# Optimization experiments

Measured on AMD Instinct MI355X. Metric: run time of the kernel, lower is better.

Reference implementation:

```python
import jax, jax.numpy as jnp
import numpy as np
from jax import lax

MIN_DELTA = 0.5 / 2 ** 3  # COMPATIBLE = False path
MAX_STEP = 20
MAX_CAMSTEP = 6
# (name, n_options, action_range_start) for non-camera discrete actions.
# range_start follows the original: commit=[0,1], camera=[1,6], then cumulative n-1.
ACTS = [("forward_back", 3, 6), ("left_right", 3, 8), ("jump", 2, 10),
        ("sneak_sprint", 4, 11), ("attack", 32, 14)]
N_ACTIONS = 45  # 6 + sum(n-1) = 6 + 39


def _forward(fc_input, camera, acts, W1, b1, W2, b2):
    B = fc_input.shape[0]
    dt = fc_input.dtype
    cam0, cam1 = camera[:, 0], camera[:, 1]
    acts = {k: v.astype(jnp.int32) for k, v in acts.items()}

    def step(carry, _):
        ac, delta, chosen, rdac, cam_steps, commited = carry
        alive = ~commited  # loss mask for this step (norm accounting in original)
        # build fc0 extra input: [current_ac(2), one-hots(44), delta(1), delta_chosen(1)]
        parts = [ac]
        for name, n, lo in ACTS:
            parts.append(jax.nn.one_hot(rdac[name], n, dtype=dt))
        step_in = jnp.concatenate(parts + [delta[:, None], chosen.astype(dt)[:, None]], axis=1)

        # ---- target dac computation (torch.no_grad block) ----
        commit = ((jnp.abs(cam0) < 1e-5) & (jnp.abs(cam1) < 1e-5)) | (cam_steps >= MAX_CAMSTEP)
        for name, n, lo in ACTS:
            commit = commit & (rdac[name] == acts[name])
        dac = jnp.zeros((B,), jnp.int32)
        modified = commit
        new_rdac = {}
        for name, n, lo in ACTS:
            a = acts[name]
            r = rdac[name]
            disc = (~modified) & (r != a)
            val = jnp.where(a == 0, r - 1 + lo, a - 1 + lo).astype(jnp.int32)
            dac = jnp.where(disc, val, dac)
            new_rdac[name] = jnp.where(disc, a, r)
            modified = modified | disc
        ac0, ac1 = ac[:, 0], ac[:, 1]
        # NOTE: original compares both camera components against ac[:, 0] (faithful).
        delta_mask = (~modified) & (~chosen) & (
            (jnp.abs(cam0 - ac0) > delta * 2.0) | (jnp.abs(cam1 - ac0) > delta * 2.0))
        dac = jnp.where(delta_mask, 5, dac)
        delta = jnp.where(delta_mask, jnp.clip(delta * 2.0, -0.5, 0.5), delta)
        modified = modified | delta_mask
        m = ~modified
        incX = cam0 >= ac0
        incY = cam1 >= ac1
        # quadrants: decX&decY->1, incX&decY->2, decX&incY->3, incX&incY->4
        dac = jnp.where(m, 1 + incX.astype(jnp.int32) + 2 * incY.astype(jnp.int32), dac)
        sx = jnp.where(incX, delta, -delta)
        sy = jnp.where(incY, delta, -delta)
        ac = jnp.stack([jnp.where(m, ac0 + sx, ac0), jnp.where(m, ac1 + sy, ac1)], axis=1)
        delta = jnp.where(m, delta * 0.5, delta)
        chosen = chosen | m
        cam_steps = cam_steps + m.astype(jnp.int32)
        commited = commited | commit
        return (ac, delta, chosen, new_rdac, cam_steps, commited), (step_in, dac, alive)

    init = (jnp.zeros((B, 2), dt),
            jnp.full((B,), MIN_DELTA, dt),
            jnp.zeros((B,), bool),
            {name: jnp.zeros((B,), jnp.int32) for name, _, _ in ACTS},
            jnp.zeros((B,), jnp.int32),
            jnp.zeros((B,), bool))
    _, (step_ins, dacs, alives) = lax.scan(step, init, None, length=MAX_STEP)
    # step_ins: [T,B,48], dacs: [T,B], alives: [T,B]
    T = MAX_STEP
    x = jnp.concatenate(
        [jnp.broadcast_to(fc_input[None], (T,) + fc_input.shape), step_ins], axis=-1)
    x = x.reshape(T * B, -1)
    h = x @ W1 + b1
    h = h * jax.nn.sigmoid(h)  # swish
    logits = h @ W2 + b2
    logp = jax.nn.log_softmax(logits, axis=-1)
    ce = -jnp.take_along_axis(logp, dacs.reshape(-1, 1), axis=1)[:, 0].reshape(T, B)
    af = alives.astype(ce.dtype)
    loss = (ce * af).sum(0) / af.sum(0)  # per-sample loss normalized by #active steps
    return loss.mean()


def setup_inputs() -> dict:
    key = jax.random.key(0)
    ks = jax.random.split(key, 10)
    B, NI, H = 4096, 1024, 2048
    D_IN = NI + 4 + 44  # 1072
    return {
        "fc_input": jax.random.normal(ks[0], (B, NI), jnp.float32),
        "camera": jax.random.normal(ks[1], (B, 2), jnp.float32),
        "forward_back": jax.random.randint(ks[2], (B,), 0, 3),
        "left_right": jax.random.randint(ks[3], (B,), 0, 3),
        "jump": jax.random.randint(ks[4], (B,), 0, 2),
        "sneak_sprint": jax.random.randint(ks[5], (B,), 0, 4),
        "attack": jax.random.randint(ks[6], (B,), 0, 32),
        "W1": jax.random.normal(ks[7], (D_IN, H), jnp.float32) * 0.02,
        "b1": jnp.zeros((H,), jnp.float32),
        "W2": jax.random.normal(ks[8], (H, N_ACTIONS), jnp.float32) * 0.02,
        "b2": jnp.zeros((N_ACTIONS,), jnp.float32),
    }


def reference(fc_input, camera, forward_back, left_right, jump, sneak_sprint, attack,
              W1, b1, W2, b2):
    acts = {"forward_back": forward_back, "left_right": left_right, "jump": jump,
            "sneak_sprint": sneak_sprint, "attack": attack}
    return _forward(fc_input, camera, acts, W1, b1, W2, b2)
```

## Files before the change

### kernel.cpp

```cpp
#include <hip/hip_runtime.h>

#define BATCH 4096
#define NI 1024
#define HID 2048
#define TSTEPS 20
#define NA 45
#define TW 512
#define SROW 520
#define MAXS 16
#define NB 4

typedef __bf16 bf16x8 __attribute__((ext_vector_type(8)));
typedef float floatx4 __attribute__((ext_vector_type(4)));

struct StepMeta {
    float ac0, ac1, delta, chosen;
    int chg;
    int dac, mult, pad;
};

__device__ __forceinline__ unsigned short f2bf(float x) {
    union { float f; unsigned int u; } un; un.f = x;
    unsigned int r = un.u + 0x7FFFu + ((un.u >> 16) & 1u);
    return (unsigned short)(r >> 16);
}

__device__ __forceinline__ float4 f4add(float4 a, float4 b) {
    return make_float4(a.x + b.x, a.y + b.y, a.z + b.z, a.w + b.w);
}

__device__ void scan_one(int b, const float* __restrict__ camera,
                         const int* __restrict__ fb_in, const int* __restrict__ lr_in,
                         const int* __restrict__ jp_in, const int* __restrict__ ss_in,
                         const int* __restrict__ at_in, StepMeta* __restrict__ meta,
                         int2* __restrict__ hdr) {
    float cam0 = camera[2 * b], cam1 = camera[2 * b + 1];
    int afb = fb_in[b], alr = lr_in[b], ajp = jp_in[b], ass = ss_in[b], aat = at_in[b];
    float ac0 = 0.f, ac1 = 0.f, delta = 0.0625f;
    int rfb = 0, rlr = 0, rjp = 0, rss = 0, rat = 0;
    bool chosen = false;
    int cam_steps = 0;
    int chgPending = -1;
    bool camzero = (fabsf(cam0) < 1e-5f) && (fabsf(cam1) < 1e-5f);
    int nd = 0, aliveTot = 0;
    float lac0 = 0.f, lac1 = 0.f, ldelta = 0.f, lchosen = 0.f;
    int ldac = -1000;
    for (int t = 0; t < TSTEPS; t++) {
        StepMeta m;
        m.ac0 = ac0; m.ac1 = ac1; m.delta = delta; m.chosen = chosen ? 1.f : 0.f;
        m.chg = chgPending; chgPending = -1;
        bool commit = (camzero || cam_steps >= 6) &&
                      rfb == afb && rlr == alr && rjp == ajp && rss == ass && rat == aat;
        int dac = 0; bool modified = commit;
        if (!modified && rfb != afb) { dac = (afb == 0 ? rfb - 1 + 6  : afb - 1 + 6 ); chgPending = ((2  + rfb) << 8) | (2  + afb); rfb = afb; modified = true; }
        if (!modified && rlr != alr) { dac = (alr == 0 ? rlr - 1 + 8  : alr - 1 + 8 ); chgPending = ((5  + rlr) << 8) | (5  + alr); rlr = alr; modified = true; }
        if (!modified && rjp != ajp) { dac = (ajp == 0 ? rjp - 1 + 10 : ajp - 1 + 10); chgPending = ((8  + rjp) << 8) | (8  + ajp); rjp = ajp; modified = true; }
        if (!modified && rss != ass) { dac = (ass == 0 ? rss - 1 + 11 : ass - 1 + 11); chgPending = ((10 + rss) << 8) | (10 + ass); rss = ass; modified = true; }
        if (!modified && rat != aat) { dac = (aat == 0 ? rat - 1 + 14 : aat - 1 + 14); chgPending = ((14 + rat) << 8) | (14 + aat); rat = aat; modified = true; }
        if (!modified && !chosen &&
            (fabsf(cam0 - ac0) > delta * 2.f || fabsf(cam1 - ac0) > delta * 2.f)) {
            dac = 5; delta = fminf(delta * 2.f, 0.5f); modified = true;
        }
        if (!modified) {
            bool incX = cam0 >= ac0, incY = cam1 >= ac1;
            dac = 1 + (incX ? 1 : 0) + (incY ? 2 : 0);
            ac0 += incX ? delta : -delta;
            ac1 += incY ? delta : -delta;
            delta *= 0.5f;
            chosen = true;
            cam_steps++;
        }
        m.dac = dac; m.mult = 1; m.pad = 0;
        if (nd > 0 && m.chg < 0 && !commit &&
            m.ac0 == lac0 && m.ac1 == lac1 && m.delta == ldelta &&
            m.chosen == lchosen && dac == ldac) {
            meta[b * MAXS + nd - 1].mult = 1 + (TSTEPS - t);
            aliveTot += (TSTEPS - t);
            break;
        }
        meta[b * MAXS + nd] = m;
        lac0 = m.ac0; lac1 = m.ac1; ldelta = m.delta; lchosen = m.chosen; ldac = dac;
        nd++; aliveTot++;
        if (commit) break;
    }
    hdr[b] = make_int2(nd, aliveTot);
}

__global__ void prep_kernel(const float* __restrict__ fc, unsigned short* __restrict__ Ab,
                            const float* __restrict__ W1, unsigned short* __restrict__ Wt,
                            const float* __restrict__ W2, unsigned short* __restrict__ W2T,
                            const float* __restrict__ camera,
                            const int* __restrict__ fb_in, const int* __restrict__ lr_in,
                            const int* __restrict__ jp_in, const int* __restrict__ ss_in,
                            const int* __restrict__ at_in, StepMeta* __restrict__ meta,
                            int2* __restrict__ hdr) {
    __shared__ float tile[32][33];
    int bid = blockIdx.x, tid = threadIdx.x;
    if (bid < 4096) {
        int idx = bid * 256 + tid;
        float4 v = ((const float4*)fc)[idx];
        ushort4 o;
        o.x = f2bf(v.x); o.y = f2bf(v.y); o.z = f2bf(v.z); o.w = f2bf(v.w);
        ((ushort4*)Ab)[idx] = o;
    } else if (bid < 6144) {
        int b2 = bid - 4096;
        int k0 = (b2 & 31) * 32, n0 = (b2 >> 5) * 32;
        int tx = tid & 31, ty = tid >> 5;
        for (int i = 0; i < 4; i++)
            tile[ty + 8 * i][tx] = W1[(size_t)(k0 + ty + 8 * i) * HID + n0 + tx];
        __syncthreads();
        for (int i = 0; i < 4; i++) {
            int n = ty + 8 * i;
            Wt[(size_t)(n0 + n) * NI + k0 + tx] = f2bf(tile[tx][n]);
        }
    } else if (bid < 6272) {
        int bid2 = bid - 6144;
        int k = bid2 * 16 + (tid >> 4);
        int nn = tid & 15;
#pragma unroll
        for (int i = 0; i < 3; i++) {
            int n = nn * 3 + i;
            W2T[(size_t)n * HID + k] = (n < NA) ? f2bf(W2[(size_t)k * NA + n]) : (unsigned short)0;
        }
    } else {
        int b = (bid - 6272) * 256 + tid;
        scan_one(b, camera, fb_in, lr_in, jp_in, ss_in, at_in, meta, hdr);
    }
}

__global__ __launch_bounds__(256) void gemm_base(const unsigned short* __restrict__ Ab,
                                                 const unsigned short* __restrict__ Wt,
                                                 const float* __restrict__ W1,
                                                 const float* __restrict__ b1,
                                                 float* __restrict__ C) {
    __shared__ __align__(16) __bf16 At[128 * 64];
    __shared__ __align__(16) __bf16 Bt[64 * 64];
    int bn = blockIdx.x, bm = blockIdx.y;
    int m0 = bm * 128, n0 = bn * 64;
    int tid = threadIdx.x;
    int wave = tid >> 6, lane = tid & 63;
    int wr = wave >> 1, wc = wave & 1;
    int l15 = lane & 15, q = lane >> 4;
    floatx4 acc[4][2];
    for (int a = 0; a < 4; a++) for (int c = 0; c < 2; c++) acc[a][c] = (floatx4){0.f, 0.f, 0.f, 0.f};
    for (int k0 = 0; k0 < NI; k0 += 64) {
        __syncthreads();
#pragma unroll
        for (int i = 0; i < 4; i++) {
            int c = i * 256 + tid;
            int row = c >> 3;
            int part = (c & 7) ^ (row & 7);
            const unsigned short* gA = &Ab[(size_t)(m0 + row) * NI + k0 + part * 8];
            __builtin_amdgcn_global_load_lds(
                (const __attribute__((address_space(1))) unsigned int*)gA,
                (__attribute__((address_space(3))) unsigned int*)&At[c * 8], 16, 0, 0);
        }
#pragma unroll
        for (int i = 0; i < 2; i++) {
            int c = i * 256 + tid;
            int row = c >> 3;
            int part = (c & 7) ^ (row & 7);
            const unsigned short* gB = &Wt[(size_t)(n0 + row) * NI + k0 + part * 8];
            __builtin_amdgcn_global_load_lds(
                (const __attribute__((address_space(1))) unsigned int*)gB,
                (__attribute__((address_space(3))) unsigned int*)&Bt[c * 8], 16, 0, 0);
        }
        __syncthreads();
#pragma unroll
        for (int ks = 0; ks < 2; ks++) {
            bf16x8 af[4], bf[2];
            for (int mr = 0; mr < 4; mr++) {
                int row = wr * 64 + mr * 16 + l15;
                int idx = (row * 64 + ks * 32 + q * 8) ^ ((row & 7) << 3);
                af[mr] = *(const bf16x8*)&At[idx];
            }
            for (int nc = 0; nc < 2; nc++) {
                int row = wc * 32 + nc * 16 + l15;
                int idx = (row * 64 + ks * 32 + q * 8) ^ ((row & 7) << 3);
                bf[nc] = *(const bf16x8*)&Bt[idx];
            }
            for (int mr = 0; mr < 4; mr++)
                for (int nc = 0; nc < 2; nc++)
                    acc[mr][nc] = __builtin_amdgcn_mfma_f32_16x16x32_bf16(af[mr], bf[nc], acc[mr][nc], 0, 0, 0);
        }
    }
    for (int nc = 0; nc < 2; nc++) {
        int col = n0 + wc * 32 + nc * 16 + l15;
        const float* We = W1 + (size_t)NI * HID + col;
        float cv = b1[col] + We[2 * HID] + We[5 * HID] + We[8 * HID] + We[10 * HID]
                 + We[14 * HID] + 0.0625f * We[46 * HID];
        for (int mr = 0; mr < 4; mr++)
            for (int r = 0; r < 4; r++) {
                int row = m0 + wr * 64 + mr * 16 + q * 4 + r;
                C[(size_t)row * HID + col] = acc[mr][nc][r] + cv;
            }
    }
}

__global__ __launch_bounds__(512, 2) void fused_mlp(const float* __restrict__ base,
                                                 const float* __restrict__ W1,
                                                 const unsigned short* __restrict__ W2T,
                                                 const float* __restrict__ b2,
                                                 const StepMeta* __restrict__ meta,
                                                 const int2* __restrict__ hdr,
                                                 float* __restrict__ loss_out) {
    __shared__ __align__(16) __bf16 S[NB * MAXS * SROW];
    __shared__ __align__(16) float4 u4s[NB][MAXS];
    __shared__ int chgs[NB][MAXS], dacsS[NB][MAXS], multsS[NB][MAXS];
    __shared__ int swapL[NB][5], nsS[NB], ndS[NB], atS[NB];
    __shared__ float b2s[48];
    __shared__ float ceArr[NB][MAXS];
    __shared__ float pmax[NB][MAXS][12], psum[NB][MAXS][12], mxS[NB][MAXS];

    int bp = blockIdx.x, tid = threadIdx.x;
    int tg = tid >> 7, tl = tid & 127;
    int wave = tid >> 6, lane = tid & 63, l15 = lane & 15, q = lane >> 4;

    if (tl == 0) {
        int2 hd = hdr[bp * NB + tg];
        ndS[tg] = hd.x; atS[tg] = hd.y;
    }
    if (tl < MAXS) {
        StepMeta m = meta[(size_t)(bp * NB + tg) * MAXS + tl];
        u4s[tg][tl] = make_float4(m.ac0, m.ac1, m.delta - 0.0625f, m.chosen);
        chgs[tg][tl] = m.chg; dacsS[tg][tl] = m.dac; multsS[tg][tl] = m.mult;
    }
    if (tid >= 64 && tid < 112) {
        int n = tid - 64;
        b2s[n] = (n < NA) ? b2[n] : 0.f;
    }
    __syncthreads();
    if (tl == 0) {
        int ns = 0, nd = ndS[tg];
        for (int s = 0; s < nd; s++)
            if (chgs[tg][s] >= 0) swapL[tg][ns++] = chgs[tg][s];
        nsS[tg] = ns;
        for (; ns < 5; ns++) swapL[tg][ns] = 0;
    }
    {
        uint4 zz = make_uint4(0, 0, 0, 0);
#pragma unroll
        for (int e = 0; e < NB; e++) {
            int nde = ndS[e];
            uint4* z = (uint4*)&S[(size_t)(e * MAXS + nde) * SROW];
            int n16 = (MAXS - nde) * 65;
            for (int i = tid; i < n16; i += 512) z[i] = zz;
        }
    }
    __syncthreads();

    const float* Wx = W1 + (size_t)NI * HID;
    const __bf16* Wb = (const __bf16*)W2T;
    floatx4 acc[4][3];
    for (int a = 0; a < 4; a++) for (int c = 0; c < 3; c++) acc[a][c] = (floatx4){0.f, 0.f, 0.f, 0.f};

    int nd = __builtin_amdgcn_readfirstlane(ndS[tg]);
    int ns = __builtin_amdgcn_readfirstlane(nsS[tg]);
    int cA = __builtin_amdgcn_readfirstlane(swapL[tg][0]);
    int cB = __builtin_amdgcn_readfirstlane(swapL[tg][1]);
    int cC = __builtin_amdgcn_readfirstlane(swapL[tg][2]);
    int cD = __builtin_amdgcn_readfirstlane(swapL[tg][3]);
    int cE = __builtin_amdgcn_readfirstlane(swapL[tg][4]);

    for (int jt = 0; jt < 4; jt++) {
        if (jt) __syncthreads();
        int j = jt * TW + 4 * tl;
        float4 w0  = *(const float4*)&Wx[j];
        float4 w1  = *(const float4*)&Wx[HID + j];
        float4 wdl = *(const float4*)&Wx[46 * HID + j];
        float4 wch = *(const float4*)&Wx[47 * HID + j];
        float4 hb  = *(const float4*)&base[(size_t)(bp * NB + tg) * HID + j];
        float4 dA = {0,0,0,0}, dB = {0,0,0,0}, dC = {0,0,0,0}, dD = {0,0,0,0}, dE = {0,0,0,0};
        if (ns > 0) { float4 n_ = *(const float4*)&Wx[(size_t)(cA & 255) * HID + j], o_ = *(const float4*)&Wx[(size_t)(cA >> 8) * HID + j];
                      dA = make_float4(n_.x - o_.x, n_.y - o_.y, n_.z - o_.z, n_.w - o_.w); }
        if (ns > 1) { float4 n_ = *(const float4*)&Wx[(size_t)(cB & 255) * HID + j], o_ = *(const float4*)&Wx[(size_t)(cB >> 8) * HID + j];
                      dB = make_float4(n_.x - o_.x, n_.y - o_.y, n_.z - o_.z, n_.w - o_.w); }
        if (ns > 2) { float4 n_ = *(const float4*)&Wx[(size_t)(cC & 255) * HID + j], o_ = *(const float4*)&Wx[(size_t)(cC >> 8) * HID + j];
                      dC = make_float4(n_.x - o_.x, n_.y - o_.y, n_.z - o_.z, n_.w - o_.w); }
        if (ns > 3) { float4 n_ = *(const float4*)&Wx[(size_t)(cD & 255) * HID + j], o_ = *(const float4*)&Wx[(size_t)(cD >> 8) * HID + j];
                      dD = make_float4(n_.x - o_.x, n_.y - o_.y, n_.z - o_.z, n_.w - o_.w); }
        if (ns > 4) { float4 n_ = *(const float4*)&Wx[(size_t)(cE & 255) * HID + j], o_ = *(const float4*)&Wx[(size_t)(cE >> 8) * HID + j];
                      dE = make_float4(n_.x - o_.x, n_.y - o_.y, n_.z - o_.z, n_.w - o_.w); }

        auto compute1 = [&](int s, float4 b) {
            float4 u = u4s[tg][s];
            float h0 = fmaf(u.w, wch.x, fmaf(u.x, w0.x, b.x)) + fmaf(u.z, wdl.x, u.y * w1.x);
            float h1 = fmaf(u.w, wch.y, fmaf(u.x, w0.y, b.y)) + fmaf(u.z, wdl.y, u.y * w1.y);
            float h2 = fmaf(u.w, wch.z, fmaf(u.x, w0.z, b.z)) + fmaf(u.z, wdl.z, u.y * w1.z);
            float h3 = fmaf(u.w, wch.w, fmaf(u.x, w0.w, b.w)) + fmaf(u.z, wdl.w, u.y * w1.w);
            float s0 = h0 * __builtin_amdgcn_rcpf(1.f + __expf(-h0));
            float s1 = h1 * __builtin_amdgcn_rcpf(1.f + __expf(-h1));
            float s2 = h2 * __builtin_amdgcn_rcpf(1.f + __expf(-h2));
            float s3 = h3 * __builtin_amdgcn_rcpf(1.f + __expf(-h3));
            union { uint2 v; __bf16 h[4]; } pk;
            pk.h[0] = (__bf16)s0; pk.h[1] = (__bf16)s1;
            pk.h[2] = (__bf16)s2; pk.h[3] = (__bf16)s3;
            *(uint2*)&S[(size_t)(tg * MAXS + s) * SROW + 4 * tl] = pk.v;
        };

        float4 sw = {0,0,0,0};
        compute1(0, hb);
        if (ns > 0) { sw = f4add(sw, dA); compute1(1, f4add(hb, sw)); }
        if (ns > 1) { sw = f4add(sw, dB); compute1(2, f4add(hb, sw)); }
        if (ns > 2) { sw = f4add(sw, dC); compute1(3, f4add(hb, sw)); }
        if (ns > 3) { sw = f4add(sw, dD); compute1(4, f4add(hb, sw)); }
        if (ns > 4) { sw = f4add(sw, dE); compute1(5, f4add(hb, sw)); }
        float4 bxv = f4add(hb, sw);
        int s = ns + 1;
        for (; s + 1 < nd; s += 2) {
            compute1(s, bxv);
            compute1(s + 1, bxv);
        }
        if (s < nd) compute1(s, bxv);

        __syncthreads();
#pragma unroll
        for (int i = 0; i < 2; i++) {
            int kc = (wave + 8 * i) * 32 + q * 8;
            bf16x8 a0 = *(const bf16x8*)&S[(size_t)l15 * SROW + kc];
            bf16x8 a1 = *(const bf16x8*)&S[(size_t)(MAXS + l15) * SROW + kc];
            bf16x8 a2 = *(const bf16x8*)&S[(size_t)(2 * MAXS + l15) * SROW + kc];
            bf16x8 a3 = *(const bf16x8*)&S[(size_t)(3 * MAXS + l15) * SROW + kc];
            int kg = jt * TW + kc;
            bf16x8 b0  = *(const bf16x8*)&Wb[(size_t)l15 * HID + kg];
            bf16x8 b1v = *(const bf16x8*)&Wb[(size_t)(16 + l15) * HID + kg];
            bf16x8 b2v = *(const bf16x8*)&Wb[(size_t)(32 + l15) * HID + kg];
            acc[0][0] = __builtin_amdgcn_mfma_f32_16x16x32_bf16(a0, b0,  acc[0][0], 0, 0, 0);
            acc[0][1] = __builtin_amdgcn_mfma_f32_16x16x32_bf16(a0, b1v, acc[0][1], 0, 0, 0);
            acc[0][2] = __builtin_amdgcn_mfma_f32_16x16x32_bf16(a0, b2v, acc[0][2], 0, 0, 0);
            acc[1][0] = __builtin_amdgcn_mfma_f32_16x16x32_bf16(a1, b0,  acc[1][0], 0, 0, 0);
            acc[1][1] = __builtin_amdgcn_mfma_f32_16x16x32_bf16(a1, b1v, acc[1][1], 0, 0, 0);
            acc[1][2] = __builtin_amdgcn_mfma_f32_16x16x32_bf16(a1, b2v, acc[1][2], 0, 0, 0);
            acc[2][0] = __builtin_amdgcn_mfma_f32_16x16x32_bf16(a2, b0,  acc[2][0], 0, 0, 0);
            acc[2][1] = __builtin_amdgcn_mfma_f32_16x16x32_bf16(a2, b1v, acc[2][1], 0, 0, 0);
            acc[2][2] = __builtin_amdgcn_mfma_f32_16x16x32_bf16(a2, b2v, acc[2][2], 0, 0, 0);
            acc[3][0] = __builtin_amdgcn_mfma_f32_16x16x32_bf16(a3, b0,  acc[3][0], 0, 0, 0);
            acc[3][1] = __builtin_amdgcn_mfma_f32_16x16x32_bf16(a3, b1v, acc[3][1], 0, 0, 0);
            acc[3][2] = __builtin_amdgcn_mfma_f32_16x16x32_bf16(a3, b2v, acc[3][2], 0, 0, 0);
        }
    }
    __syncthreads();
    float* logitsP = (float*)S;
    float* logitsF = (float*)S + 12288;
    if (wave >= 4) {
        int wv = wave - 4;
#pragma unroll
        for (int e = 0; e < 4; e++)
#pragma unroll
            for (int nt = 0; nt < 3; nt++)
#pragma unroll
                for (int r = 0; r < 4; r++)
                    logitsP[(size_t)(wv * 4 + e) * 768 + (q * 4 + r) * 48 + nt * 16 + l15] = acc[e][nt][r];
    }
    __syncthreads();
    if (wave < 4) {
        int wv = wave;
#pragma unroll
        for (int e = 0; e < 4; e++)
#pragma unroll
            for (int nt = 0; nt < 3; nt++)
#pragma unroll
                for (int r = 0; r < 4; r++) {
                    size_t idx = (size_t)(wv * 4 + e) * 768 + (q * 4 + r) * 48 + nt * 16 + l15;
                    logitsP[idx] += acc[e][nt][r];
                }
    }
    __syncthreads();
    for (int i = tid; i < 768; i += 512) {
        int e = i / 192, rem = i - e * 192;
        int row = rem / 12, gE = rem - row * 12;
        const float4* P0 = (const float4*)(logitsP + (size_t)(0 * 4 + e) * 768);
        const float4* P1 = (const float4*)(logitsP + (size_t)(1 * 4 + e) * 768);
        const float4* P2 = (const float4*)(logitsP + (size_t)(2 * 4 + e) * 768);
        const float4* P3 = (const float4*)(logitsP + (size_t)(3 * 4 + e) * 768);
        float4 p0 = P0[rem], p1 = P1[rem], p2 = P2[rem], p3 = P3[rem];
        float4 bb = *(const float4*)&b2s[gE * 4];
        float4 r;
        r.x = p0.x + p1.x + p2.x + p3.x + bb.x;
        r.y = p0.y + p1.y + p2.y + p3.y + bb.y;
        r.z = p0.z + p1.z + p2.z + p3.z + bb.z;
        r.w = p0.w + p1.w + p2.w + p3.w + bb.w;
        ((float4*)(logitsF + (size_t)e * 768))[rem] = r;
        float lm = (gE == 11) ? r.x : fmaxf(fmaxf(r.x, r.y), fmaxf(r.z, r.w));
        pmax[e][row][gE] = lm;
    }
    __syncthreads();
    if (tid < 64) {
        int e = tid >> 4, row = tid & 15;
        float m = pmax[e][row][0];
        for (int i = 1; i < 12; i++) m = fmaxf(m, pmax[e][row][i]);
        mxS[e][row] = m;
    }
    __syncthreads();
    for (int i = tid; i < 768; i += 512) {
        int e = i / 192, rem = i - e * 192;
        int row = rem / 12, gE = rem - row * 12;
        float m = mxS[e][row];
        float4 v = ((const float4*)(logitsF + (size_t)e * 768))[rem];
        float s;
        if (gE == 11) s = __expf(v.x - m);
        else s = __expf(v.x - m) + __expf(v.y - m) + __expf(v.z - m) + __expf(v.w - m);
        psum[e][row][gE] = s;
    }
    __syncthreads();
    if (tl < nd) {
        float ssum = 0.f;
        for (int i = 0; i < 12; i++) ssum += psum[tg][tl][i];
        float m = mxS[tg][tl];
        int dac = dacsS[tg][tl];
        float ld = logitsF[(size_t)tg * 768 + tl * 48 + dac];
        float ce = -(ld - m - logf(ssum));
        ceArr[tg][tl] = ce * (float)multsS[tg][tl];
    }
    __syncthreads();
    if (tl == 0) {
        float s = 0.f;
        for (int t = 0; t < nd; t++) s += ceArr[tg][t];
        loss_out[bp * NB + tg] = s / (float)atS[tg];
    }
}

__global__ __launch_bounds__(512) void reduce_loss(const float* __restrict__ loss,
                                                   float* __restrict__ out) {
    int tid = threadIdx.x;
    const float4* l4 = (const float4*)loss;
    float4 a = l4[tid];
    float4 b = l4[512 + tid];
    float s = (a.x + a.y + a.z + a.w) + (b.x + b.y + b.z + b.w);
    for (int off = 32; off > 0; off >>= 1) s += __shfl_down(s, off, 64);
    __shared__ float wsum[8];
    if ((tid & 63) == 0) wsum[tid >> 6] = s;
    __syncthreads();
    if (tid == 0) {
        float t = 0.f;
        for (int i = 0; i < 8; i++) t += wsum[i];
        out[0] = t * (1.0f / (float)BATCH);
    }
}

extern "C" void kernel_launch(void* const* d_in, const int* in_sizes, int n_in,
                              void* d_out, int out_size, void* d_ws, size_t ws_size,
                              hipStream_t stream) {
    const float* fc_input = (const float*)d_in[0];
    const float* camera   = (const float*)d_in[1];
    const int*   fb       = (const int*)d_in[2];
    const int*   lr       = (const int*)d_in[3];
    const int*   jp       = (const int*)d_in[4];
    const int*   ss       = (const int*)d_in[5];
    const int*   at       = (const int*)d_in[6];
    const float* W1       = (const float*)d_in[7];
    const float* b1       = (const float*)d_in[8];
    const float* W2       = (const float*)d_in[9];
    const float* b2       = (const float*)d_in[10];
    float* out = (float*)d_out;

    char* ws = (char*)d_ws;
    unsigned short* Ab   = (unsigned short*)(ws);
    unsigned short* Wt   = (unsigned short*)(ws + 8388608);
    float*          baseB= (float*)(ws + 12582912);
    StepMeta*       meta = (StepMeta*)(ws + 46137344);
    int2*           hdr  = (int2*)(ws + 48234496);
    float*          lossB= (float*)(ws + 48267264);
    unsigned short* W2T  = (unsigned short*)(ws + 48283648);

    prep_kernel<<<4096 + 2048 + 128 + 16, 256, 0, stream>>>(fc_input, Ab, W1, Wt, W2, W2T,
                                                            camera, fb, lr, jp, ss, at, meta, hdr);
    gemm_base<<<dim3(HID / 64, BATCH / 128), 256, 0, stream>>>(Ab, Wt, W1, b1, baseB);
    fused_mlp<<<BATCH / NB, 512, 0, stream>>>(baseB, W1, W2T, b2, meta, hdr, lossB);
    reduce_loss<<<1, 512, 0, stream>>>(lossB, out);
}
```

Measured before the change: 192.8 us.

## Process eight batch elements per block to amortize W2 loads

Doubles the number of batch elements handled per fused_mlp block from 4 to 8. Each thread group now builds hidden activations for two elements, and every W2T fragment loaded from global memory feeds 8 element tiles of MFMAs instead of 4. This halves the grid size and W2/W1-extra reloads per element, at the cost of doubled LDS use, more accumulator registers, and dropping to one block per CU via launch bounds.

```diff
diff --git a/kernel.cpp b/kernel.cpp
--- a/kernel.cpp
+++ b/kernel.cpp
@@ -8,7 +8,7 @@
 #define TW 512
 #define SROW 520
 #define MAXS 16
-#define NB 4
+#define NB 8
 
 typedef __bf16 bf16x8 __attribute__((ext_vector_type(8)));
 typedef float floatx4 __attribute__((ext_vector_type(4)));
@@ -197,7 +197,7 @@
     }
 }
 
-__global__ __launch_bounds__(512, 2) void fused_mlp(const float* __restrict__ base,
+__global__ __launch_bounds__(512, 1) void fused_mlp(const float* __restrict__ base,
                                                  const float* __restrict__ W1,
                                                  const unsigned short* __restrict__ W2T,
                                                  const float* __restrict__ b2,
@@ -213,30 +213,32 @@
     __shared__ float pmax[NB][MAXS][12], psum[NB][MAXS][12], mxS[NB][MAXS];
 
     int bp = blockIdx.x, tid = threadIdx.x;
-    int tg = tid >> 7, tl = tid & 127;
+    int cg = tid >> 7, ctl = tid & 127;
     int wave = tid >> 6, lane = tid & 63, l15 = lane & 15, q = lane >> 4;
 
-    if (tl == 0) {
-        int2 hd = hdr[bp * NB + tg];
-        ndS[tg] = hd.x; atS[tg] = hd.y;
-    }
-    if (tl < MAXS) {
-        StepMeta m = meta[(size_t)(bp * NB + tg) * MAXS + tl];
-        u4s[tg][tl] = make_float4(m.ac0, m.ac1, m.delta - 0.0625f, m.chosen);
-        chgs[tg][tl] = m.chg; dacsS[tg][tl] = m.dac; multsS[tg][tl] = m.mult;
+    if (tid < NB) {
+        int2 hd = hdr[bp * NB + tid];
+        ndS[tid] = hd.x; atS[tid] = hd.y;
+    }
+    if (tid >= 128 && tid < 128 + NB * MAXS) {
+        int e = (tid - 128) >> 4, s = (tid - 128) & 15;
+        StepMeta m = meta[(size_t)(bp * NB + e) * MAXS + s];
+        u4s[e][s] = make_float4(m.ac0, m.ac1, m.delta - 0.0625f, m.chosen);
+        chgs[e][s] = m.chg; dacsS[e][s] = m.dac; multsS[e][s] = m.mult;
     }
     if (tid >= 64 && tid < 112) {
         int n = tid - 64;
         b2s[n] = (n < NA) ? b2[n] : 0.f;
     }
     __syncthreads();
-    if (tl == 0) {
-        int ns = 0, nd = ndS[tg];
+    if (tid < NB) {
+        int ns = 0, nd = ndS[tid];
         for (int s = 0; s < nd; s++)
-            if (chgs[tg][s] >= 0) swapL[tg][ns++] = chgs[tg][s];
-        nsS[tg] = ns;
-        for (; ns < 5; ns++) swapL[tg][ns] = 0;
-    }
+            if (chgs[tid][s] >= 0) swapL[tid][ns++] = chgs[tid][s];
+        nsS[tid] = ns;
+        for (; ns < 5; ns++) swapL[tid][ns] = 0;
+    }
+    __syncthreads();
     {
         uint4 zz = make_uint4(0, 0, 0, 0);
 #pragma unroll
@@ -251,39 +253,30 @@
 
     const float* Wx = W1 + (size_t)NI * HID;
     const __bf16* Wb = (const __bf16*)W2T;
-    floatx4 acc[4][3];
-    for (int a = 0; a < 4; a++) for (int c = 0; c < 3; c++) acc[a][c] = (floatx4){0.f, 0.f, 0.f, 0.f};
-
-    int nd = __builtin_amdgcn_readfirstlane(ndS[tg]);
-    int ns = __builtin_amdgcn_readfirstlane(nsS[tg]);
-    int cA = __builtin_amdgcn_readfirstlane(swapL[tg][0]);
-    int cB = __builtin_amdgcn_readfirstlane(swapL[tg][1]);
-    int cC = __builtin_amdgcn_readfirstlane(swapL[tg][2]);
-    int cD = __builtin_amdgcn_readfirstlane(swapL[tg][3]);
-    int cE = __builtin_amdgcn_readfirstlane(swapL[tg][4]);
+    floatx4 acc[NB][3];
+    for (int a = 0; a < NB; a++) for (int c = 0; c < 3; c++) acc[a][c] = (floatx4){0.f, 0.f, 0.f, 0.f};
+
+    int ndA0 = __builtin_amdgcn_readfirstlane(ndS[2 * cg]);
+    int ndA1 = __builtin_amdgcn_readfirstlane(ndS[2 * cg + 1]);
+    int nsA0 = __builtin_amdgcn_readfirstlane(nsS[2 * cg]);
+    int nsA1 = __builtin_amdgcn_readfirstlane(nsS[2 * cg + 1]);
+    int cL0[5], cL1[5];
+#pragma unroll
+    for (int k = 0; k < 5; k++) {
+        cL0[k] = __builtin_amdgcn_readfirstlane(swapL[2 * cg][k]);
+        cL1[k] = __builtin_amdgcn_readfirstlane(swapL[2 * cg + 1][k]);
+    }
 
     for (int jt = 0; jt < 4; jt++) {
         if (jt) __syncthreads();
-        int j = jt * TW + 4 * tl;
+        int j = jt * TW + 4 * ctl;
         float4 w0  = *(const float4*)&Wx[j];
         float4 w1  = *(const float4*)&Wx[HID + j];
         float4 wdl = *(const float4*)&Wx[46 * HID + j];
         float4 wch = *(const float4*)&Wx[47 * HID + j];
-        float4 hb  = *(const float4*)&base[(size_t)(bp * NB + tg) * HID + j];
-        float4 dA = {0,0,0,0}, dB = {0,0,0,0}, dC = {0,0,0,0}, dD = {0,0,0,0}, dE = {0,0,0,0};
-        if (ns > 0) { float4 n_ = *(const float4*)&Wx[(size_t)(cA & 255) * HID + j], o_ = *(const float4*)&Wx[(size_t)(cA >> 8) * HID + j];
-                      dA = make_float4(n_.x - o_.x, n_.y - o_.y, n_.z - o_.z, n_.w - o_.w); }
-        if (ns > 1) { float4 n_ = *(const float4*)&Wx[(size_t)(cB & 255) * HID + j], o_ = *(const float4*)&Wx[(size_t)(cB >> 8) * HID + j];
-                      dB = make_float4(n_.x - o_.x, n_.y - o_.y, n_.z - o_.z, n_.w - o_.w); }
-        if (ns > 2) { float4 n_ = *(const float4*)&Wx[(size_t)(cC & 255) * HID + j], o_ = *(const float4*)&Wx[(size_t)(cC >> 8) * HID + j];
-                      dC = make_float4(n_.x - o_.x, n_.y - o_.y, n_.z - o_.z, n_.w - o_.w); }
-        if (ns > 3) { float4 n_ = *(const float4*)&Wx[(size_t)(cD & 255) * HID + j], o_ = *(const float4*)&Wx[(size_t)(cD >> 8) * HID + j];
-                      dD = make_float4(n_.x - o_.x, n_.y - o_.y, n_.z - o_.z, n_.w - o_.w); }
-        if (ns > 4) { float4 n_ = *(const float4*)&Wx[(size_t)(cE & 255) * HID + j], o_ = *(const float4*)&Wx[(size_t)(cE >> 8) * HID + j];
-                      dE = make_float4(n_.x - o_.x, n_.y - o_.y, n_.z - o_.z, n_.w - o_.w); }
-
-        auto compute1 = [&](int s, float4 b) {
-            float4 u = u4s[tg][s];
+
+        auto compute1 = [&](int e, int s, float4 b) {
+            float4 u = u4s[e][s];
             float h0 = fmaf(u.w, wch.x, fmaf(u.x, w0.x, b.x)) + fmaf(u.z, wdl.x, u.y * w1.x);
             float h1 = fmaf(u.w, wch.y, fmaf(u.x, w0.y, b.y)) + fmaf(u.z, wdl.y, u.y * w1.y);
             float h2 = fmaf(u.w, wch.z, fmaf(u.x, w0.z, b.z)) + fmaf(u.z, wdl.z, u.y * w1.z);
@@ -295,84 +288,88 @@
             union { uint2 v; __bf16 h[4]; } pk;
             pk.h[0] = (__bf16)s0; pk.h[1] = (__bf16)s1;
             pk.h[2] = (__bf16)s2; pk.h[3] = (__bf16)s3;
-            *(uint2*)&S[(size_t)(tg * MAXS + s) * SROW + 4 * tl] = pk.v;
+            *(uint2*)&S[(size_t)(e * MAXS + s) * SROW + 4 * ctl] = pk.v;
         };
 
-        float4 sw = {0,0,0,0};
-        compute1(0, hb);
-        if (ns > 0) { sw = f4add(sw, dA); compute1(1, f4add(hb, sw)); }
-        if (ns > 1) { sw = f4add(sw, dB); compute1(2, f4add(hb, sw)); }
-        if (ns > 2) { sw = f4add(sw, dC); compute1(3, f4add(hb, sw)); }
-        if (ns > 3) { sw = f4add(sw, dD); compute1(4, f4add(hb, sw)); }
-        if (ns > 4) { sw = f4add(sw, dE); compute1(5, f4add(hb, sw)); }
-        float4 bxv = f4add(hb, sw);
-        int s = ns + 1;
-        for (; s + 1 < nd; s += 2) {
-            compute1(s, bxv);
-            compute1(s + 1, bxv);
-        }
-        if (s < nd) compute1(s, bxv);
+        auto doElem = [&](int e, int ns_, int nd_, const int* cL) {
+            float4 hb = *(const float4*)&base[(size_t)(bp * NB + e) * HID + j];
+            float4 d0 = {0,0,0,0}, d1 = {0,0,0,0}, d2 = {0,0,0,0}, d3 = {0,0,0,0}, d4 = {0,0,0,0};
+            if (ns_ > 0) { float4 n_ = *(const float4*)&Wx[(size_t)(cL[0] & 255) * HID + j], o_ = *(const float4*)&Wx[(size_t)(cL[0] >> 8) * HID + j];
+                           d0 = make_float4(n_.x - o_.x, n_.y - o_.y, n_.z - o_.z, n_.w - o_.w); }
+            if (ns_ > 1) { float4 n_ = *(const float4*)&Wx[(size_t)(cL[1] & 255) * HID + j], o_ = *(const float4*)&Wx[(size_t)(cL[1] >> 8) * HID + j];
+                           d1 = make_float4(n_.x - o_.x, n_.y - o_.y, n_.z - o_.z, n_.w - o_.w); }
+            if (ns_ > 2) { float4 n_ = *(const float4*)&Wx[(size_t)(cL[2] & 255) * HID + j], o_ = *(const float4*)&Wx[(size_t)(cL[2] >> 8) * HID + j];
+                           d2 = make_float4(n_.x - o_.x, n_.y - o_.y, n_.z - o_.z, n_.w - o_.w); }
+            if (ns_ > 3) { float4 n_ = *(const float4*)&Wx[(size_t)(cL[3] & 255) * HID + j], o_ = *(const float4*)&Wx[(size_t)(cL[3] >> 8) * HID + j];
+                           d3 = make_float4(n_.x - o_.x, n_.y - o_.y, n_.z - o_.z, n_.w - o_.w); }
+            if (ns_ > 4) { float4 n_ = *(const float4*)&Wx[(size_t)(cL[4] & 255) * HID + j], o_ = *(const float4*)&Wx[(size_t)(cL[4] >> 8) * HID + j];
+                           d4 = make_float4(n_.x - o_.x, n_.y - o_.y, n_.z - o_.z, n_.w - o_.w); }
+            float4 sw = {0,0,0,0};
+            compute1(e, 0, hb);
+            if (ns_ > 0) { sw = f4add(sw, d0); compute1(e, 1, f4add(hb, sw)); }
+            if (ns_ > 1) { sw = f4add(sw, d1); compute1(e, 2, f4add(hb, sw)); }
+            if (ns_ > 2) { sw = f4add(sw, d2); compute1(e, 3, f4add(hb, sw)); }
+            if (ns_ > 3) { sw = f4add(sw, d3); compute1(e, 4, f4add(hb, sw)); }
+            if (ns_ > 4) { sw = f4add(sw, d4); compute1(e, 5, f4add(hb, sw)); }
+            float4 bxv = f4add(hb, sw);
+            int s = ns_ + 1;
+            for (; s + 1 < nd_; s += 2) { compute1(e, s, bxv); compute1(e, s + 1, bxv); }
+            if (s < nd_) compute1(e, s, bxv);
+        };
+        doElem(2 * cg,     nsA0, ndA0, cL0);
+        doElem(2 * cg + 1, nsA1, ndA1, cL1);
 
         __syncthreads();
 #pragma unroll
         for (int i = 0; i < 2; i++) {
             int kc = (wave + 8 * i) * 32 + q * 8;
-            bf16x8 a0 = *(const bf16x8*)&S[(size_t)l15 * SROW + kc];
-            bf16x8 a1 = *(const bf16x8*)&S[(size_t)(MAXS + l15) * SROW + kc];
-            bf16x8 a2 = *(const bf16x8*)&S[(size_t)(2 * MAXS + l15) * SROW + kc];
-            bf16x8 a3 = *(const bf16x8*)&S[(size_t)(3 * MAXS + l15) * SROW + kc];
             int kg = jt * TW + kc;
             bf16x8 b0  = *(const bf16x8*)&Wb[(size_t)l15 * HID + kg];
             bf16x8 b1v = *(const bf16x8*)&Wb[(size_t)(16 + l15) * HID + kg];
             bf16x8 b2v = *(const bf16x8*)&Wb[(size_t)(32 + l15) * HID + kg];
-            acc[0][0] = __builtin_amdgcn_mfma_f32_16x16x32_bf16(a0, b0,  acc[0][0], 0, 0, 0);
-            acc[0][1] = __builtin_amdgcn_mfma_f32_16x16x32_bf16(a0, b1v, acc[0][1], 0, 0, 0);
-            acc[0][2] = __builtin_amdgcn_mfma_f32_16x16x32_bf16(a0, b2v, acc[0][2], 0, 0, 0);
-            acc[1][0] = __builtin_amdgcn_mfma_f32_16x16x32_bf16(a1, b0,  acc[1][0], 0, 0, 0);
-            acc[1][1] = __builtin_amdgcn_mfma_f32_16x16x32_bf16(a1, b1v, acc[1][1], 0, 0, 0);
-            acc[1][2] = __builtin_amdgcn_mfma_f32_16x16x32_bf16(a1, b2v, acc[1][2], 0, 0, 0);
-            acc[2][0] = __builtin_amdgcn_mfma_f32_16x16x32_bf16(a2, b0,  acc[2][0], 0, 0, 0);
-            acc[2][1] = __builtin_amdgcn_mfma_f32_16x16x32_bf16(a2, b1v, acc[2][1], 0, 0, 0);
-            acc[2][2] = __builtin_amdgcn_mfma_f32_16x16x32_bf16(a2, b2v, acc[2][2], 0, 0, 0);
-            acc[3][0] = __builtin_amdgcn_mfma_f32_16x16x32_bf16(a3, b0,  acc[3][0], 0, 0, 0);
-            acc[3][1] = __builtin_amdgcn_mfma_f32_16x16x32_bf16(a3, b1v, acc[3][1], 0, 0, 0);
-            acc[3][2] = __builtin_amdgcn_mfma_f32_16x16x32_bf16(a3, b2v, acc[3][2], 0, 0, 0);
+#pragma unroll
+            for (int e = 0; e < NB; e++) {
+                bf16x8 a = *(const bf16x8*)&S[(size_t)(e * MAXS + l15) * SROW + kc];
+                acc[e][0] = __builtin_amdgcn_mfma_f32_16x16x32_bf16(a, b0,  acc[e][0], 0, 0, 0);
+                acc[e][1] = __builtin_amdgcn_mfma_f32_16x16x32_bf16(a, b1v, acc[e][1], 0, 0, 0);
+                acc[e][2] = __builtin_amdgcn_mfma_f32_16x16x32_bf16(a, b2v, acc[e][2], 0, 0, 0);
+            }
         }
     }
     __syncthreads();
     float* logitsP = (float*)S;
-    float* logitsF = (float*)S + 12288;
+    float* logitsF = (float*)S + 24576;
     if (wave >= 4) {
         int wv = wave - 4;
 #pragma unroll
-        for (int e = 0; e < 4; e++)
+        for (int e = 0; e < NB; e++)
 #pragma unroll
             for (int nt = 0; nt < 3; nt++)
 #pragma unroll
                 for (int r = 0; r < 4; r++)
-                    logitsP[(size_t)(wv * 4 + e) * 768 + (q * 4 + r) * 48 + nt * 16 + l15] = acc[e][nt][r];
+                    logitsP[(size_t)(wv * NB + e) * 768 + (q * 4 + r) * 48 + nt * 16 + l15] = acc[e][nt][r];
     }
     __syncthreads();
     if (wave < 4) {
         int wv = wave;
 #pragma unroll
-        for (int e = 0; e < 4; e++)
+        for (int e = 0; e < NB; e++)
 #pragma unroll
             for (int nt = 0; nt < 3; nt++)
 #pragma unroll
                 for (int r = 0; r < 4; r++) {
-                    size_t idx = (size_t)(wv * 4 + e) * 768 + (q * 4 + r) * 48 + nt * 16 + l15;
+                    size_t idx = (size_t)(wv * NB + e) * 768 + (q * 4 + r) * 48 + nt * 16 + l15;
                     logitsP[idx] += acc[e][nt][r];
                 }
     }
     __syncthreads();
-    for (int i = tid; i < 768; i += 512) {
+    for (int i = tid; i < NB * 192; i += 512) {
         int e = i / 192, rem = i - e * 192;
         int row = rem / 12, gE = rem - row * 12;
-        const float4* P0 = (const float4*)(logitsP + (size_t)(0 * 4 + e) * 768);
-        const float4* P1 = (const float4*)(logitsP + (size_t)(1 * 4 + e) * 768);
-        const float4* P2 = (const float4*)(logitsP + (size_t)(2 * 4 + e) * 768);
-        const float4* P3 = (const float4*)(logitsP + (size_t)(3 * 4 + e) * 768);
+        const float4* P0 = (const float4*)(logitsP + (size_t)(0 * NB + e) * 768);
+        const float4* P1 = (const float4*)(logitsP + (size_t)(1 * NB + e) * 768);
+        const float4* P2 = (const float4*)(logitsP + (size_t)(2 * NB + e) * 768);
+        const float4* P3 = (const float4*)(logitsP + (size_t)(3 * NB + e) * 768);
         float4 p0 = P0[rem], p1 = P1[rem], p2 = P2[rem], p3 = P3[rem];
         float4 bb = *(const float4*)&b2s[gE * 4];
         float4 r;
@@ -385,14 +382,14 @@
         pmax[e][row][gE] = lm;
     }
     __syncthreads();
-    if (tid < 64) {
+    if (tid < NB * MAXS) {
         int e = tid >> 4, row = tid & 15;
         float m = pmax[e][row][0];
         for (int i = 1; i < 12; i++) m = fmaxf(m, pmax[e][row][i]);
         mxS[e][row] = m;
     }
     __syncthreads();
-    for (int i = tid; i < 768; i += 512) {
+    for (int i = tid; i < NB * 192; i += 512) {
         int e = i / 192, rem = i - e * 192;
         int row = rem / 12, gE = rem - row * 12;
         float m = mxS[e][row];
@@ -403,20 +400,24 @@
         psum[e][row][gE] = s;
     }
     __syncthreads();
-    if (tl < nd) {
-        float ssum = 0.f;
-        for (int i = 0; i < 12; i++) ssum += psum[tg][tl][i];
-        float m = mxS[tg][tl];
-        int dac = dacsS[tg][tl];
-        float ld = logitsF[(size_t)tg * 768 + tl * 48 + dac];
-        float ce = -(ld - m - logf(ssum));
-        ceArr[tg][tl] = ce * (float)multsS[tg][tl];
-    }
-    __syncthreads();
-    if (tl == 0) {
-        float s = 0.f;
-        for (int t = 0; t < nd; t++) s += ceArr[tg][t];
-        loss_out[bp * NB + tg] = s / (float)atS[tg];
+    {
+        int tg8 = tid >> 6, tl8 = tid & 63;
+        int ndE = __builtin_amdgcn_readfirstlane(ndS[tg8]);
+        if (tl8 < ndE) {
+            float ssum = 0.f;
+            for (int i = 0; i < 12; i++) ssum += psum[tg8][tl8][i];
+            float m = mxS[tg8][tl8];
+            int dac = dacsS[tg8][tl8];
+            float ld = logitsF[(size_t)tg8 * 768 + tl8 * 48 + dac];
+            float ce = -(ld - m - logf(ssum));
+            ceArr[tg8][tl8] = ce * (float)multsS[tg8][tl8];
+        }
+        __syncthreads();
+        if (tl8 == 0) {
+            float s = 0.f;
+            for (int t = 0; t < ndE; t++) s += ceArr[tg8][t];
+            loss_out[bp * NB + tg8] = s / (float)atS[tg8];
+        }
     }
 }
 
```

New measurement: 203.5 us. 1.06x slower.
